# Performance work log

Measured on AMD Instinct MI355X. Metric: run time of the kernel, lower is better.

## Reference

```python
import jax, jax.numpy as jnp
import numpy as np

INPUT_DIM = 22
HIDDEN_DIM = 9
TAGSET_SIZE = 4
SEQ_LEN = 524288


def setup_inputs() -> dict:
    key = jax.random.key(0)
    ks = jax.random.split(key, 7)
    s = 1.0 / np.sqrt(HIDDEN_DIM)  # PyTorch LSTM/Linear default init scale
    x = jax.random.normal(ks[0], (SEQ_LEN, INPUT_DIM), dtype=jnp.float32)
    w_ih = jax.random.uniform(ks[1], (4 * HIDDEN_DIM, INPUT_DIM), jnp.float32, -s, s)
    w_hh = jax.random.uniform(ks[2], (4 * HIDDEN_DIM, HIDDEN_DIM), jnp.float32, -s, s)
    b_ih = jax.random.uniform(ks[3], (4 * HIDDEN_DIM,), jnp.float32, -s, s)
    b_hh = jax.random.uniform(ks[4], (4 * HIDDEN_DIM,), jnp.float32, -s, s)
    w_out = jax.random.uniform(ks[5], (TAGSET_SIZE, HIDDEN_DIM), jnp.float32, -s, s)
    b_out = jax.random.uniform(ks[6], (TAGSET_SIZE,), jnp.float32, -s, s)
    return {"input_sequence": x, "w_ih": w_ih, "w_hh": w_hh, "b_ih": b_ih,
            "b_hh": b_hh, "w_out": w_out, "b_out": b_out}


def reference(input_sequence, w_ih, w_hh, b_ih, b_hh, w_out, b_out):
    H = w_hh.shape[1]
    # Precompute input contribution to gates for all timesteps: [S, 4H]
    x_gates = input_sequence @ w_ih.T + (b_ih + b_hh)

    def step(carry, xg):
        h, c = carry
        gates = xg + h @ w_hh.T  # [4H], PyTorch gate order: i, f, g, o
        i = jax.nn.sigmoid(gates[0 * H:1 * H])
        f = jax.nn.sigmoid(gates[1 * H:2 * H])
        g = jnp.tanh(gates[2 * H:3 * H])
        o = jax.nn.sigmoid(gates[3 * H:4 * H])
        c_new = f * c + i * g
        h_new = o * jnp.tanh(c_new)
        return (h_new, c_new), h_new

    h0 = jnp.zeros((H,), dtype=input_sequence.dtype)
    c0 = jnp.zeros((H,), dtype=input_sequence.dtype)
    _, hs = jax.lax.scan(step, (h0, c0), x_gates)  # hs: [S, H]

    tag_space = hs @ w_out.T + b_out  # [S, tagset_size]
    return jax.nn.log_softmax(tag_space, axis=1)
```

## Files before the change

kernel.cpp:

```cpp
#include <hip/hip_runtime.h>

#define S_LEN   524288
#define IN_D    22
#define HID     9
#define NTAG    4
#define CHUNK   128
#define BURN    64
#define NCHUNK  (S_LEN / CHUNK)
#define WPB     4
#define TILE    16
#define ROWF    24
#define TILEF   (TILE * ROWF)
#define NLOADS  (TILEF / 64)

__device__ __forceinline__ float qrot1(float v) {
  return __int_as_float(__builtin_amdgcn_update_dpp(
      0, __float_as_int(v), 0x39 , 0xF, 0xF, true));
}
__device__ __forceinline__ float qxor1(float v) {
  return __int_as_float(__builtin_amdgcn_update_dpp(
      0, __float_as_int(v), 0xB1 , 0xF, 0xF, true));
}
__device__ __forceinline__ float qxor2(float v) {
  return __int_as_float(__builtin_amdgcn_update_dpp(
      0, __float_as_int(v), 0x4E , 0xF, 0xF, true));
}

__global__ __launch_bounds__(256, 4)
void lstm_chunk_scan(const float* __restrict__ x,
                     const float* __restrict__ w_ih,
                     const float* __restrict__ w_hh,
                     const float* __restrict__ b_ih,
                     const float* __restrict__ b_hh,
                     const float* __restrict__ w_out,
                     const float* __restrict__ b_out,
                     float* __restrict__ out)
{
  __shared__ __align__(16) float lds[WPB * 2 * TILEF];

  const int tid  = threadIdx.x;
  const int wv   = __builtin_amdgcn_readfirstlane(tid >> 6);
  const int lane = tid & 63;
  const int u    = lane >> 2;
  const int g    = lane & 3;
  const bool act = (u < HID);
  const int row  = act ? (g * HID + u) : 0;

  float wih[IN_D], whh[HID], wo[HID];
#pragma unroll
  for (int k = 0; k < IN_D; ++k) wih[k] = act ? w_ih[row * IN_D + k] : 0.f;
#pragma unroll
  for (int k = 0; k < HID; ++k)  whh[k] = act ? w_hh[row * HID + k] : 0.f;
  const float bias = act ? (b_ih[row] + b_hh[row]) : 0.f;
  const int orow = (lane < NTAG) ? lane : 0;
  float wo_b = b_out[orow];
#pragma unroll
  for (int k = 0; k < HID; ++k)  wo[k] = w_out[orow * HID + k];
  if (lane >= NTAG) { wo_b = 0.f; }

  const float mexp = (g == 2) ? -2.885390082f : -1.442695041f;
  const float smul = (g == 2) ? 2.f : 1.f;
  const float soff = (g == 2) ? -1.f : 0.f;

  const int chunk = __builtin_amdgcn_readfirstlane((int)blockIdx.x * WPB + wv);
  const int start = chunk * CHUNK;
  const int t0    = (start >= BURN) ? (start - BURN) : 0;
  const int nstep = start + CHUNK - t0;
  const int ntile = nstep / TILE;

  float* myl = lds + wv * 2 * TILEF;

  int goff[NLOADS];
#pragma unroll
  for (int cc = 0; cc < NLOADS; ++cc) {
    int slot = cc * 64 + lane;
    int r = slot / ROWF;
    int col = slot - r * ROWF;
    if (col >= IN_D) col = IN_D - 1;
    goff[cc] = r * IN_D + col;
  }
  const long XMAX = (long)S_LEN * IN_D - 1;

  float stage[NLOADS];
  {
    long tb = (long)t0 * IN_D;
#pragma unroll
    for (int cc = 0; cc < NLOADS; ++cc) {
      long gi = tb + goff[cc];
      if (gi > XMAX) gi = XMAX;
      stage[cc] = x[gi];
    }
#pragma unroll
    for (int cc = 0; cc < NLOADS; ++cc) myl[cc * 64 + lane] = stage[cc];
  }

  float sh[HID];
#pragma unroll
  for (int k = 0; k < HID; ++k) sh[k] = 0.f;
  float cst = 0.f;

  for (int ti = 0; ti < ntile; ++ti) {
    {
      long tb = (long)(t0 + (ti + 1) * TILE) * IN_D;
#pragma unroll
      for (int cc = 0; cc < NLOADS; ++cc) {
        long gi = tb + goff[cc];
        if (gi > XMAX) gi = XMAX;
        stage[cc] = x[gi];
      }
    }

    const float* rb = myl + (ti & 1) * TILEF;
    const int tbase = t0 + ti * TILE;
    const bool outp = (tbase >= start);

#pragma unroll
    for (int s = 0; s < TILE; ++s) {
      const float* xr = rb + s * ROWF;
      float xv[22];
      *(float4*)(&xv[0])  = *(const float4*)(xr + 0);
      *(float4*)(&xv[4])  = *(const float4*)(xr + 4);
      *(float4*)(&xv[8])  = *(const float4*)(xr + 8);
      *(float4*)(&xv[12]) = *(const float4*)(xr + 12);
      *(float4*)(&xv[16]) = *(const float4*)(xr + 16);
      *(float2*)(&xv[20]) = *(const float2*)(xr + 20);

      float a0 = bias, a1 = 0.f;
#pragma unroll
      for (int k = 0; k < IN_D; ++k) {
        if (k & 1) a1 = fmaf(xv[k], wih[k], a1);
        else       a0 = fmaf(xv[k], wih[k], a0);
      }
#pragma unroll
      for (int k = 0; k < HID; ++k) {
        if (k & 1) a1 = fmaf(sh[k], whh[k], a1);
        else       a0 = fmaf(sh[k], whh[k], a0);
      }
      float pre = a0 + a1;

      float ex = __builtin_amdgcn_exp2f(pre * mexp);
      float gv = fmaf(__builtin_amdgcn_rcpf(1.f + ex), smul, soff);

      float fg = qrot1(gv);
      float gg = qrot1(fg);
      float og = qrot1(gg);
      cst = fmaf(fg, cst, gv * gg);
      float e2 = __builtin_amdgcn_exp2f(cst * -2.885390082f);
      float th = fmaf(__builtin_amdgcn_rcpf(1.f + e2), 2.f, -1.f);
      float hv = og * th;

#pragma unroll
      for (int k = 0; k < HID; ++k)
        sh[k] = __int_as_float(
            __builtin_amdgcn_readlane(__float_as_int(hv), 4 * k));

      if (outp) {
        float acc = wo_b;
#pragma unroll
        for (int k = 0; k < HID; ++k) acc = fmaf(sh[k], wo[k], acc);
        float m = fmaxf(acc, qxor1(acc));
        m = fmaxf(m, qxor2(m));
        float xm = acc - m;
        float ee = __builtin_amdgcn_exp2f(xm * 1.442695041f);
        float sm = ee + qxor1(ee);
        sm = sm + qxor2(sm);
        float res = fmaf(-0.69314718056f, __builtin_amdgcn_logf(sm), xm);
        if (lane < NTAG) out[(long)(tbase + s) * NTAG + lane] = res;
      }
    }

    float* wb = myl + ((ti + 1) & 1) * TILEF;
#pragma unroll
    for (int cc = 0; cc < NLOADS; ++cc) wb[cc * 64 + lane] = stage[cc];
  }
}

extern "C" void kernel_launch(void* const* d_in, const int* in_sizes, int n_in,
                              void* d_out, int out_size, void* d_ws, size_t ws_size,
                              hipStream_t stream) {
  (void)in_sizes; (void)n_in; (void)d_ws; (void)ws_size; (void)out_size;
  const float* x     = (const float*)d_in[0];
  const float* w_ih  = (const float*)d_in[1];
  const float* w_hh  = (const float*)d_in[2];
  const float* b_ih  = (const float*)d_in[3];
  const float* b_hh  = (const float*)d_in[4];
  const float* w_out = (const float*)d_in[5];
  const float* b_out = (const float*)d_in[6];
  float* out = (float*)d_out;

  hipLaunchKernelGGL(lstm_chunk_scan, dim3(NCHUNK / WPB), dim3(256), 0, stream,
                     x, w_ih, w_hh, b_ih, b_hh, w_out, b_out, out);
}
```

Before: 186.3 us.

## Split LSTM into input-GEMM, recurrent scan, and output-head kernels via fp16 workspace

Splits the fused kernel into three launches. The first precomputes input gate pre-activations for all timesteps into an fp16 workspace, with the exp scale folded into the weights. The second runs the chunked recurrent scan, reading only the precomputed gates and writing fp16 hidden states. The third computes the output projection and log-softmax in parallel. The goal is to take the 22-wide input dot product and the head off the serial critical path, at the cost of extra global traffic, fp16 rounding and two extra launches. The old fused kernel is kept as a fallback when the workspace is too small.

```diff
diff --git a/kernel.cpp b/kernel.cpp
--- a/kernel.cpp
+++ b/kernel.cpp
@@ -1,4 +1,5 @@
 #include <hip/hip_runtime.h>
+#include <hip/hip_fp16.h>
 
 #define S_LEN   524288
 #define IN_D    22
@@ -8,23 +9,154 @@
 #define BURN    64
 #define NCHUNK  (S_LEN / CHUNK)
 #define WPB     4
+#define PF      8
+#define GT      8
+
+#define XGP_HALFS ((size_t)S_LEN * 36)
+#define H_HALFS   ((size_t)S_LEN * HID)
+#define WS_NEED   ((XGP_HALFS + H_HALFS) * 2)
+
+template <int PAT>
+__device__ __forceinline__ float qperm(float v) {
+  return __int_as_float(__builtin_amdgcn_update_dpp(
+      0, __float_as_int(v), PAT, 0xF, 0xF, true));
+}
+
+__global__ __launch_bounds__(256)
+void xg_gemm(const float* __restrict__ x, const float* __restrict__ w_ih,
+             const float* __restrict__ b_ih, const float* __restrict__ b_hh,
+             __half* __restrict__ xgp)
+{
+  const int tid = (int)blockIdx.x * 256 + threadIdx.x;
+  const int t8  = tid / 36;
+  const int l   = tid - t8 * 36;
+  const int u = l >> 2, g = l & 3, row = g * HID + u;
+  const float mex = (g == 2) ? -2.885390082f : -1.442695041f;
+
+  float wr[IN_D];
+#pragma unroll
+  for (int k = 0; k < IN_D; ++k) wr[k] = w_ih[row * IN_D + k] * mex;
+  const float bb = (b_ih[row] + b_hh[row]) * mex;
+
+  const long tb = (long)t8 * GT;
+#pragma unroll
+  for (int j = 0; j < GT; ++j) {
+    const float* xr = x + (tb + j) * IN_D;
+    float xv[IN_D];
+#pragma unroll
+    for (int c = 0; c < IN_D / 2; ++c)
+      *(float2*)(&xv[2 * c]) = *(const float2*)(xr + 2 * c);
+    float a0 = bb, a1 = 0.f;
+#pragma unroll
+    for (int k = 0; k < IN_D; ++k) {
+      if (k & 1) a1 = fmaf(xv[k], wr[k], a1);
+      else       a0 = fmaf(xv[k], wr[k], a0);
+    }
+    xgp[(tb + j) * 36 + l] = __float2half(a0 + a1);
+  }
+}
+
+__global__ __launch_bounds__(256, 4)
+void lstm_scan2(const __half* __restrict__ xgp,
+                const float* __restrict__ w_hh,
+                __half* __restrict__ hout)
+{
+  const int tid  = threadIdx.x;
+  const int wv   = tid >> 6;
+  const int lane = tid & 63;
+  const int u = lane >> 2, g = lane & 3;
+  const bool act = (u < HID);
+  const int row  = act ? (g * HID + u) : 0;
+  const long ll  = (lane < 36) ? lane : 35;
+  const float mexp = (g == 2) ? -2.885390082f : -1.442695041f;
+  const float smul = (g == 2) ? 2.f : 1.f;
+  const float soff = (g == 2) ? -1.f : 0.f;
+
+  float whh[HID];
+#pragma unroll
+  for (int k = 0; k < HID; ++k)
+    whh[k] = (act ? w_hh[row * HID + k] : 0.f) * mexp;
+
+  const int chunk = (int)blockIdx.x * WPB + wv;
+  const int start = chunk * CHUNK;
+  const int t0    = (start >= BURN) ? (start - BURN) : 0;
+  const int nstep = start + CHUNK - t0;
+
+  __half xq[PF];
+#pragma unroll
+  for (int j = 0; j < PF; ++j) xq[j] = xgp[(long)(t0 + j) * 36 + ll];
+
+  float sh[HID];
+#pragma unroll
+  for (int k = 0; k < HID; ++k) sh[k] = 0.f;
+  float cst = 0.f;
+
+  for (int b = 0; b < nstep / PF; ++b) {
+    const int tb = t0 + b * PF;
+    const bool outp = (tb >= start);
+#pragma unroll
+    for (int j = 0; j < PF; ++j) {
+      float a0 = __half2float(xq[j]);
+      {
+        long tt = tb + j + PF; if (tt >= S_LEN) tt = S_LEN - 1;
+        xq[j] = xgp[tt * 36 + ll];
+      }
+      float a1 = 0.f;
+#pragma unroll
+      for (int k = 0; k < HID; ++k) {
+        if (k & 1) a1 = fmaf(sh[k], whh[k], a1);
+        else       a0 = fmaf(sh[k], whh[k], a0);
+      }
+      const float pre = a0 + a1;
+      const float ex  = __builtin_amdgcn_exp2f(pre);
+      const float gv  = fmaf(__builtin_amdgcn_rcpf(1.f + ex), smul, soff);
+
+      const float fg = qperm<0x39>(gv);
+      const float gg = qperm<0x4E>(gv);
+      const float og = qperm<0x93>(gv);
+      cst = fmaf(fg, cst, gv * gg);
+      const float e2 = __builtin_amdgcn_exp2f(cst * -2.885390082f);
+      const float th = fmaf(__builtin_amdgcn_rcpf(1.f + e2), 2.f, -1.f);
+      const float hv = og * th;
+
+#pragma unroll
+      for (int k = 0; k < HID; ++k)
+        sh[k] = __int_as_float(
+            __builtin_amdgcn_readlane(__float_as_int(hv), 4 * k));
+
+      if (outp && g == 0 && u < HID)
+        hout[(long)(tb + j) * HID + u] = __float2half(hv);
+    }
+  }
+}
+
+__global__ __launch_bounds__(256)
+void head_k(const __half* __restrict__ h, const float* __restrict__ w_out,
+            const float* __restrict__ b_out, float* __restrict__ out)
+{
+  const int tid = (int)blockIdx.x * 256 + threadIdx.x;
+  const int t = tid >> 2, tag = tid & 3;
+  float wo[HID];
+#pragma unroll
+  for (int k = 0; k < HID; ++k) wo[k] = w_out[tag * HID + k];
+  float acc = b_out[tag];
+  const __half* hr = h + (long)t * HID;
+#pragma unroll
+  for (int k = 0; k < HID; ++k) acc = fmaf(__half2float(hr[k]), wo[k], acc);
+
+  float m = fmaxf(acc, qperm<0xB1>(acc));
+  m = fmaxf(m, qperm<0x4E>(m));
+  const float xm = acc - m;
+  const float ee = __builtin_amdgcn_exp2f(xm * 1.442695041f);
+  float sm = ee + qperm<0xB1>(ee);
+  sm = sm + qperm<0x4E>(sm);
+  out[tid] = fmaf(-0.69314718056f, __builtin_amdgcn_logf(sm), xm);
+}
+
 #define TILE    16
 #define ROWF    24
 #define TILEF   (TILE * ROWF)
 #define NLOADS  (TILEF / 64)
-
-__device__ __forceinline__ float qrot1(float v) {
-  return __int_as_float(__builtin_amdgcn_update_dpp(
-      0, __float_as_int(v), 0x39 , 0xF, 0xF, true));
-}
-__device__ __forceinline__ float qxor1(float v) {
-  return __int_as_float(__builtin_amdgcn_update_dpp(
-      0, __float_as_int(v), 0xB1 , 0xF, 0xF, true));
-}
-__device__ __forceinline__ float qxor2(float v) {
-  return __int_as_float(__builtin_amdgcn_update_dpp(
-      0, __float_as_int(v), 0x4E , 0xF, 0xF, true));
-}
 
 __global__ __launch_bounds__(256, 4)
 void lstm_chunk_scan(const float* __restrict__ x,
@@ -141,9 +273,9 @@
       float ex = __builtin_amdgcn_exp2f(pre * mexp);
       float gv = fmaf(__builtin_amdgcn_rcpf(1.f + ex), smul, soff);
 
-      float fg = qrot1(gv);
-      float gg = qrot1(fg);
-      float og = qrot1(gg);
+      float fg = qperm<0x39>(gv);
+      float gg = qperm<0x4E>(gv);
+      float og = qperm<0x93>(gv);
       cst = fmaf(fg, cst, gv * gg);
       float e2 = __builtin_amdgcn_exp2f(cst * -2.885390082f);
       float th = fmaf(__builtin_amdgcn_rcpf(1.f + e2), 2.f, -1.f);
@@ -158,12 +290,12 @@
         float acc = wo_b;
 #pragma unroll
         for (int k = 0; k < HID; ++k) acc = fmaf(sh[k], wo[k], acc);
-        float m = fmaxf(acc, qxor1(acc));
-        m = fmaxf(m, qxor2(m));
+        float m = fmaxf(acc, qperm<0xB1>(acc));
+        m = fmaxf(m, qperm<0x4E>(m));
         float xm = acc - m;
         float ee = __builtin_amdgcn_exp2f(xm * 1.442695041f);
-        float sm = ee + qxor1(ee);
-        sm = sm + qxor2(sm);
+        float sm = ee + qperm<0xB1>(ee);
+        sm = sm + qperm<0x4E>(sm);
         float res = fmaf(-0.69314718056f, __builtin_amdgcn_logf(sm), xm);
         if (lane < NTAG) out[(long)(tbase + s) * NTAG + lane] = res;
       }
@@ -178,7 +310,7 @@
 extern "C" void kernel_launch(void* const* d_in, const int* in_sizes, int n_in,
                               void* d_out, int out_size, void* d_ws, size_t ws_size,
                               hipStream_t stream) {
-  (void)in_sizes; (void)n_in; (void)d_ws; (void)ws_size; (void)out_size;
+  (void)in_sizes; (void)n_in; (void)out_size;
   const float* x     = (const float*)d_in[0];
   const float* w_ih  = (const float*)d_in[1];
   const float* w_hh  = (const float*)d_in[2];
@@ -188,6 +320,17 @@
   const float* b_out = (const float*)d_in[6];
   float* out = (float*)d_out;
 
-  hipLaunchKernelGGL(lstm_chunk_scan, dim3(NCHUNK / WPB), dim3(256), 0, stream,
-                     x, w_ih, w_hh, b_ih, b_hh, w_out, b_out, out);
-}
+  if (ws_size >= WS_NEED) {
+    __half* xgp = (__half*)d_ws;
+    __half* h   = (__half*)d_ws + XGP_HALFS;
+    hipLaunchKernelGGL(xg_gemm, dim3(36 * (S_LEN / GT) / 256), dim3(256), 0,
+                       stream, x, w_ih, b_ih, b_hh, xgp);
+    hipLaunchKernelGGL(lstm_scan2, dim3(NCHUNK / WPB), dim3(256), 0, stream,
+                       xgp, w_hh, h);
+    hipLaunchKernelGGL(head_k, dim3(S_LEN * NTAG / 256), dim3(256), 0, stream,
+                       h, w_out, b_out, out);
+  } else {
+    hipLaunchKernelGGL(lstm_chunk_scan, dim3(NCHUNK / WPB), dim3(256), 0,
+                       stream, x, w_ih, w_hh, b_ih, b_hh, w_out, b_out, out);
+  }
+}
```

Result: slower. 215.4 us (+15.6%).
